# Optimization experiments

Hardware: AMD Instinct MI355X
Metric: run time of the kernel (lower is better)

The kernel has to match this reference:

```python
import jax, jax.numpy as jnp
import numpy as np

WS = 16      # window size
NH = 8       # num heads
LN_EPS = 1e-5
F_NORM_EPS = 1e-12  # torch F.normalize eps


def layer_norm(x, w, b):
    mu = jnp.mean(x, axis=-1, keepdims=True)
    var = jnp.mean((x - mu) ** 2, axis=-1, keepdims=True)
    return (x - mu) / jnp.sqrt(var + LN_EPS) * w + b


def setup_inputs() -> dict:
    key = jax.random.key(0)
    ks = jax.random.split(key, 8)
    b, h, w, c = 2, 192, 192, 128
    n = WS * WS
    x = jax.random.normal(ks[0], (b, h * w, c), dtype=jnp.float32)
    rpi = jax.random.randint(ks[1], (n, n), 0, (2 * WS - 1) ** 2)
    s = 0.02
    inp = {
        'x': x,
        'qkv_w': jax.random.normal(ks[2], (c, 3 * c), jnp.float32) * s,
        'qkv_b': jnp.zeros((3 * c,), jnp.float32),
        'proj_w': jax.random.normal(ks[3], (c, c), jnp.float32) * s,
        'proj_b': jnp.zeros((c,), jnp.float32),
        'logit_scale': jnp.full((NH, 1, 1), jnp.log(10.0), jnp.float32),
        'rpb_table': jax.random.normal(ks[4], ((2 * WS - 1) ** 2, NH), jnp.float32) * s,
        'norm1_w': jnp.ones((c,), jnp.float32),
        'norm1_b': jnp.zeros((c,), jnp.float32),
        'norm2_w': jnp.ones((c,), jnp.float32),
        'norm2_b': jnp.zeros((c,), jnp.float32),
        'fc1_w': jax.random.normal(ks[5], (c, 2 * c), jnp.float32) * s,
        'fc1_b': jnp.zeros((2 * c,), jnp.float32),
        'fc2_w': jax.random.normal(ks[6], (2 * c, c), jnp.float32) * s,
        'fc2_b': jnp.zeros((c,), jnp.float32),
        'h': h,
        'w': w,
        'rpi': rpi,
    }
    return inp


def reference(x, qkv_w, qkv_b, proj_w, proj_b, logit_scale, rpb_table,
              norm1_w, norm1_b, norm2_w, norm2_b, fc1_w, fc1_b, fc2_w, fc2_b,
              h, w, rpi):
    b, L, c = x.shape
    ws, nh = WS, NH
    d = c // nh
    n = ws * ws
    shortcut = x

    # window partition: (b, h, w, c) -> (b*nW, ws*ws, c)
    xi = x.reshape(b, h // ws, ws, w // ws, ws, c)
    xw = xi.transpose(0, 1, 3, 2, 4, 5).reshape(-1, n, c)

    # cosine window attention (SwinV2 style)
    qkv = (xw @ qkv_w + qkv_b).reshape(-1, n, 3, nh, d).transpose(2, 0, 3, 1, 4)
    q, k, v = qkv[0], qkv[1], qkv[2]                       # (B_, nh, n, d)
    qn = q / jnp.maximum(jnp.linalg.norm(q, axis=-1, keepdims=True), F_NORM_EPS)
    kn = k / jnp.maximum(jnp.linalg.norm(k, axis=-1, keepdims=True), F_NORM_EPS)
    scale = jnp.exp(jnp.minimum(logit_scale, jnp.log(100.0)))  # (nh,1,1)
    attn = jnp.einsum('bhnd,bhmd->bhnm', qn, kn) * scale
    bias = rpb_table[rpi.reshape(-1)].reshape(n, n, nh).transpose(2, 0, 1)
    attn = jax.nn.softmax(attn + bias[None], axis=-1)
    out = jnp.einsum('bhnm,bhmd->bhnd', attn, v)
    out = out.transpose(0, 2, 1, 3).reshape(-1, n, c) @ proj_w + proj_b

    # window reverse
    xr = out.reshape(b, h // ws, w // ws, ws, ws, c)
    xr = xr.transpose(0, 1, 3, 2, 4, 5).reshape(b, L, c)

    # res-post-norm residual + MLP (GELU), eval mode (no dropout/drop_path)
    x1 = shortcut + layer_norm(xr, norm1_w, norm1_b)
    y = jax.nn.gelu(x1 @ fc1_w + fc1_b, approximate=False) @ fc2_w + fc2_b
    return x1 + layer_norm(y, norm2_w, norm2_b)
```

## Files before the change

kernel.cpp:

```cpp
#include <hip/hip_runtime.h>
#include <hip/hip_bf16.h>
#include <math.h>

#define BB 2
#define HH 192
#define WW 192
#define CC 128
#define LL (HH*WW)
#define WSZ 16
#define NTOK 256
#define NHEAD 8
#define DHEAD 16
#define NWS 12
#define NWB 144
#define NWT 288
#define MT (BB*LL)

#define OFF_BIAS   0
#define OFF_QKV    262144
#define OFF_ATTN   14417920
#define OFF_X1     19136512
#define OFF_X1B    28573696
#define OFF_HID    33292288
#define OFF_WT     42729472
#define WT_QKV 0
#define WT_PROJ 49152
#define WT_FC1 65536
#define WT_FC2 98304

typedef short  bf16x8 __attribute__((ext_vector_type(8)));
typedef float  f32x4  __attribute__((ext_vector_type(4)));
#define MFMA16(a,b,c) __builtin_amdgcn_mfma_f32_16x16x32_bf16(a,b,c,0,0,0)

__device__ __forceinline__ ushort f2b(float f) {
    uint u = __float_as_uint(f);
    uint r = u + 0x7fffu + ((u >> 16) & 1u);
    return (ushort)(r >> 16);
}
__device__ __forceinline__ float b2f(ushort u) {
    return __uint_as_float(((uint)u) << 16);
}

__device__ __forceinline__ int win_to_g(int wi, int t) {
    int b   = wi / NWB;
    int win = wi - b*NWB;
    int hi  = win / NWS;
    int wj  = win - hi*NWS;
    return b*LL + (hi*WSZ + (t >> 4))*WW + wj*WSZ + (t & 15);
}

__global__ __launch_bounds__(256) void bias_kernel(const int* __restrict__ rpi,
                                                   const float* __restrict__ rpb,
                                                   ushort* __restrict__ biasT) {
    int gid = blockIdx.x*256 + threadIdx.x;
    int j = gid >> 8, i = gid & 255;
    int idx = rpi[i*256 + j];
    #pragma unroll
    for (int h = 0; h < 8; ++h)
        biasT[h*65536 + j*256 + i] = f2b(rpb[idx*8 + h]);
}

__global__ __launch_bounds__(256) void wconv_kernel(const float* __restrict__ qkv_w,
                                                    const float* __restrict__ proj_w,
                                                    const float* __restrict__ fc1_w,
                                                    const float* __restrict__ fc2_w,
                                                    ushort* __restrict__ wt) {
    int gid = blockIdx.x*256 + threadIdx.x;
    if (gid < 49152) {
        int n = gid >> 7, k = gid & 127;
        wt[gid] = f2b(qkv_w[k*384 + n]);
    } else if (gid < 65536) {
        int i = gid - 49152; int n = i >> 7, k = i & 127;
        wt[gid] = f2b(proj_w[k*128 + n]);
    } else if (gid < 98304) {
        int i = gid - 65536; int n = i >> 7, k = i & 127;
        wt[gid] = f2b(fc1_w[k*256 + n]);
    } else {
        int i = gid - 98304; int n = i >> 8, k = i & 255;
        wt[gid] = f2b(fc2_w[k*128 + n]);
    }
}

__global__ __launch_bounds__(256) void qkv_mfma(const float* __restrict__ x,
                                                const ushort* __restrict__ wt,
                                                const float* __restrict__ wb,
                                                const float* __restrict__ lscale,
                                                ushort* __restrict__ qkvbuf) {
    __shared__ ushort alds[128][136];
    const int tid = threadIdx.x;
    const int wi  = blockIdx.x >> 1;
    const int t0w = (blockIdx.x & 1) << 7;
    #pragma unroll
    for (int it = 0; it < 16; ++it) {
        int idx = it*256 + tid;
        int row = idx >> 5, c4 = idx & 31;
        int g = win_to_g(wi, t0w + row);
        float4 v = ((const float4*)x)[g*32 + c4];
        ushort4 b;
        b.x = f2b(v.x); b.y = f2b(v.y); b.z = f2b(v.z); b.w = f2b(v.w);
        *(ushort4*)&alds[row][c4*4] = b;
    }
    __syncthreads();
    const int wv = tid >> 6, lane = tid & 63;
    const int lr = lane & 15, kg = lane >> 4;
    bf16x8 af[2][4];
    #pragma unroll
    for (int mt = 0; mt < 2; ++mt)
        #pragma unroll
        for (int ks = 0; ks < 4; ++ks)
            af[mt][ks] = *(const bf16x8*)&alds[wv*32 + mt*16 + lr][ks*32 + kg*8];

    #pragma unroll 4
    for (int t = 0; t < 24; ++t) {
        bf16x8 bfr[4];
        #pragma unroll
        for (int ks = 0; ks < 4; ++ks)
            bfr[ks] = *(const bf16x8*)(wt + (t*16 + lr)*128 + ks*32 + kg*8);
        f32x4 acc[2];
        acc[0] = (f32x4)0.f; acc[1] = (f32x4)0.f;
        #pragma unroll
        for (int mt = 0; mt < 2; ++mt)
            #pragma unroll
            for (int ks = 0; ks < 4; ++ks)
                acc[mt] = MFMA16(af[mt][ks], bfr[ks], acc[mt]);

        const int s = t >> 3, head = t & 7;
        const float bcol = wb[s*128 + head*16 + lr];
        #pragma unroll
        for (int mt = 0; mt < 2; ++mt)
            #pragma unroll
            for (int r = 0; r < 4; ++r) acc[mt][r] += bcol;
        if (s < 2) {
            float sc = (s == 0) ? __expf(fminf(lscale[head], 4.6051701860f)) : 1.f;
            #pragma unroll
            for (int mt = 0; mt < 2; ++mt)
                #pragma unroll
                for (int r = 0; r < 4; ++r) {
                    float ss = acc[mt][r]*acc[mt][r];
                    ss += __shfl_xor(ss, 1);
                    ss += __shfl_xor(ss, 2);
                    ss += __shfl_xor(ss, 4);
                    ss += __shfl_xor(ss, 8);
                    acc[mt][r] *= sc / fmaxf(sqrtf(ss), 1e-12f);
                }
        }
        ushort* dst = qkvbuf + ((wi*8+head)*3 + s)*4096;
        #pragma unroll
        for (int mt = 0; mt < 2; ++mt)
            #pragma unroll
            for (int r = 0; r < 4; ++r) {
                int row = t0w + wv*32 + mt*16 + kg*4 + r;
                dst[row*16 + lr] = f2b(acc[mt][r]);
            }
    }
}

__global__ __launch_bounds__(256) void attn_mfma(const ushort* __restrict__ qkv,
                                                 const ushort* __restrict__ biasT,
                                                 ushort* __restrict__ attn_o) {
    __shared__ ushort Vt[16][256];
    __shared__ ushort Plds[4][64][72];
    const int tid = threadIdx.x;
    const int wi = blockIdx.x >> 3, head = blockIdx.x & 7;
    const ushort* qb = qkv + ((wi*8 + head)*3)*4096;
    const ushort* kb = qb + 4096;
    const ushort* vb = qb + 8192;
    {
        const ushort* vr = vb + tid*16;
        #pragma unroll
        for (int c = 0; c < 4; ++c) {
            ushort4 vv = *(const ushort4*)(vr + c*4);
            Vt[c*4+0][tid] = vv.x; Vt[c*4+1][tid] = vv.y;
            Vt[c*4+2][tid] = vv.z; Vt[c*4+3][tid] = vv.w;
        }
    }
    const int wv = tid >> 6, lane = tid & 63;
    const int lr = lane & 15, kg = lane >> 4;
    bf16x8 qf[4];
    #pragma unroll
    for (int mt = 0; mt < 4; ++mt)
        qf[mt] = (kg < 2) ? *(const bf16x8*)(qb + (wv*64 + mt*16 + lr)*16 + kg*8)
                          : (bf16x8)0;
    __syncthreads();

    f32x4 oacc[4];
    #pragma unroll
    for (int mt = 0; mt < 4; ++mt) oacc[mt] = (f32x4)0.f;
    float lsum[4][4];
    #pragma unroll
    for (int mt = 0; mt < 4; ++mt)
        #pragma unroll
        for (int r = 0; r < 4; ++r) lsum[mt][r] = 0.f;

    for (int jt = 0; jt < 4; ++jt) {
        bf16x8 kf[4];
        #pragma unroll
        for (int nt = 0; nt < 4; ++nt)
            kf[nt] = (kg < 2) ? *(const bf16x8*)(kb + (jt*64 + nt*16 + lr)*16 + kg*8)
                              : (bf16x8)0;
        #pragma unroll
        for (int nt = 0; nt < 4; ++nt) {
            f32x4 s[4];
            #pragma unroll
            for (int mt = 0; mt < 4; ++mt)
                s[mt] = MFMA16(qf[mt], kf[nt], (f32x4)0.f);
            const int key = jt*64 + nt*16 + lr;
            #pragma unroll
            for (int mt = 0; mt < 4; ++mt) {
                ushort4 bb = *(const ushort4*)(biasT + head*65536 + key*256
                                               + wv*64 + mt*16 + kg*4);
                float p0 = __expf(s[mt][0] + b2f(bb.x));
                float p1 = __expf(s[mt][1] + b2f(bb.y));
                float p2 = __expf(s[mt][2] + b2f(bb.z));
                float p3 = __expf(s[mt][3] + b2f(bb.w));
                lsum[mt][0] += p0; lsum[mt][1] += p1;
                lsum[mt][2] += p2; lsum[mt][3] += p3;
                Plds[wv][mt*16 + kg*4 + 0][nt*16 + lr] = f2b(p0);
                Plds[wv][mt*16 + kg*4 + 1][nt*16 + lr] = f2b(p1);
                Plds[wv][mt*16 + kg*4 + 2][nt*16 + lr] = f2b(p2);
                Plds[wv][mt*16 + kg*4 + 3][nt*16 + lr] = f2b(p3);
            }
        }
        #pragma unroll
        for (int kt = 0; kt < 2; ++kt) {
            bf16x8 vf = *(const bf16x8*)&Vt[lr][jt*64 + kt*32 + kg*8];
            #pragma unroll
            for (int mt = 0; mt < 4; ++mt) {
                bf16x8 pf = *(const bf16x8*)&Plds[wv][mt*16 + lr][kt*32 + kg*8];
                oacc[mt] = MFMA16(pf, vf, oacc[mt]);
            }
        }
    }
    #pragma unroll
    for (int mt = 0; mt < 4; ++mt) {
        #pragma unroll
        for (int r = 0; r < 4; ++r) {
            float v = lsum[mt][r];
            v += __shfl_xor(v, 1);
            v += __shfl_xor(v, 2);
            v += __shfl_xor(v, 4);
            v += __shfl_xor(v, 8);
            lsum[mt][r] = 1.f / v;
        }
    }
    #pragma unroll
    for (int mt = 0; mt < 4; ++mt) {
        #pragma unroll
        for (int r = 0; r < 4; ++r) {
            int q = wv*64 + mt*16 + kg*4 + r;
            attn_o[(wi*256 + q)*128 + head*16 + lr] = f2b(oacc[mt][r] * lsum[mt][r]);
        }
    }
}

__global__ __launch_bounds__(256) void proj_mfma(const ushort* __restrict__ a,
                                                 const ushort* __restrict__ wt,
                                                 const float* __restrict__ wb,
                                                 const float* __restrict__ x,
                                                 const float* __restrict__ n1w,
                                                 const float* __restrict__ n1b,
                                                 float* __restrict__ x1,
                                                 ushort* __restrict__ x1b) {
    __shared__ ushort alds[128][136];
    const int tid = threadIdx.x;
    const int M0 = blockIdx.x * 128;
    #pragma unroll
    for (int it = 0; it < 16; ++it) {
        int idx = it*256 + tid;
        int row = idx >> 5, c4 = idx & 31;
        *(ushort4*)&alds[row][c4*4] = ((const ushort4*)a)[M0*32 + idx];
    }
    __syncthreads();
    const int wv = tid >> 6, lane = tid & 63;
    const int lr = lane & 15, kg = lane >> 4;
    bf16x8 af[2][4];
    #pragma unroll
    for (int mt = 0; mt < 2; ++mt)
        #pragma unroll
        for (int ks = 0; ks < 4; ++ks)
            af[mt][ks] = *(const bf16x8*)&alds[wv*32 + mt*16 + lr][ks*32 + kg*8];

    f32x4 acc[2][8];
    #pragma unroll
    for (int mt = 0; mt < 2; ++mt)
        #pragma unroll
        for (int t = 0; t < 8; ++t) acc[mt][t] = (f32x4)0.f;
    #pragma unroll
    for (int t = 0; t < 8; ++t) {
        bf16x8 bfr[4];
        #pragma unroll
        for (int ks = 0; ks < 4; ++ks)
            bfr[ks] = *(const bf16x8*)(wt + (t*16 + lr)*128 + ks*32 + kg*8);
        #pragma unroll
        for (int mt = 0; mt < 2; ++mt)
            #pragma unroll
            for (int ks = 0; ks < 4; ++ks)
                acc[mt][t] = MFMA16(af[mt][ks], bfr[ks], acc[mt][t]);
    }
    #pragma unroll
    for (int t = 0; t < 8; ++t) {
        float bcol = wb[t*16 + lr];
        #pragma unroll
        for (int mt = 0; mt < 2; ++mt)
            #pragma unroll
            for (int r = 0; r < 4; ++r) acc[mt][t][r] += bcol;
    }
    float mu_[2][4], rs_[2][4];
    #pragma unroll
    for (int mt = 0; mt < 2; ++mt)
        #pragma unroll
        for (int r = 0; r < 4; ++r) {
            float s = 0.f, q = 0.f;
            #pragma unroll
            for (int t = 0; t < 8; ++t) { float v = acc[mt][t][r]; s += v; q += v*v; }
            s += __shfl_xor(s,1); q += __shfl_xor(q,1);
            s += __shfl_xor(s,2); q += __shfl_xor(q,2);
            s += __shfl_xor(s,4); q += __shfl_xor(q,4);
            s += __shfl_xor(s,8); q += __shfl_xor(q,8);
            float mu = s*(1.f/128.f);
            float var = q*(1.f/128.f) - mu*mu;
            mu_[mt][r] = mu; rs_[mt][r] = rsqrtf(var + 1e-5f);
        }
    float w1c[8], b1c[8];
    #pragma unroll
    for (int t = 0; t < 8; ++t) { w1c[t] = n1w[t*16+lr]; b1c[t] = n1b[t*16+lr]; }
    #pragma unroll
    for (int mt = 0; mt < 2; ++mt)
        #pragma unroll
        for (int r = 0; r < 4; ++r) {
            int M = M0 + wv*32 + mt*16 + kg*4 + r;
            int g = win_to_g(M >> 8, M & 255);
            #pragma unroll
            for (int t = 0; t < 8; ++t) {
                int col = t*16 + lr;
                float val = x[g*128 + col]
                          + (acc[mt][t][r]-mu_[mt][r])*rs_[mt][r]*w1c[t] + b1c[t];
                x1[g*128 + col] = val;
                x1b[g*128 + col] = f2b(val);
            }
        }
}

__global__ __launch_bounds__(256) void fc1_mfma(const ushort* __restrict__ a,
                                                const ushort* __restrict__ wt,
                                                const float* __restrict__ wb,
                                                ushort* __restrict__ hidden) {
    __shared__ ushort alds[128][136];
    const int tid = threadIdx.x;
    const int M0 = blockIdx.x * 128;
    #pragma unroll
    for (int it = 0; it < 16; ++it) {
        int idx = it*256 + tid;
        int row = idx >> 5, c4 = idx & 31;
        *(ushort4*)&alds[row][c4*4] = ((const ushort4*)a)[M0*32 + idx];
    }
    __syncthreads();
    const int wv = tid >> 6, lane = tid & 63;
    const int lr = lane & 15, kg = lane >> 4;
    bf16x8 af[2][4];
    #pragma unroll
    for (int mt = 0; mt < 2; ++mt)
        #pragma unroll
        for (int ks = 0; ks < 4; ++ks)
            af[mt][ks] = *(const bf16x8*)&alds[wv*32 + mt*16 + lr][ks*32 + kg*8];

    #pragma unroll 4
    for (int t = 0; t < 16; ++t) {
        bf16x8 bfr[4];
        #pragma unroll
        for (int ks = 0; ks < 4; ++ks)
            bfr[ks] = *(const bf16x8*)(wt + (t*16 + lr)*128 + ks*32 + kg*8);
        f32x4 acc[2];
        acc[0] = (f32x4)0.f; acc[1] = (f32x4)0.f;
        #pragma unroll
        for (int mt = 0; mt < 2; ++mt)
            #pragma unroll
            for (int ks = 0; ks < 4; ++ks)
                acc[mt] = MFMA16(af[mt][ks], bfr[ks], acc[mt]);
        float bcol = wb[t*16 + lr];
        int col = t*16 + lr;
        #pragma unroll
        for (int mt = 0; mt < 2; ++mt)
            #pragma unroll
            for (int r = 0; r < 4; ++r) {
                int row = M0 + wv*32 + mt*16 + kg*4 + r;
                float v = acc[mt][r] + bcol;
                float gl = v*0.5f*(1.f + erff(v*0.70710678118654752f));
                hidden[row*256 + col] = f2b(gl);
            }
    }
}

__global__ __launch_bounds__(256) void fc2_mfma(const ushort* __restrict__ a,
                                                const ushort* __restrict__ wt,
                                                const float* __restrict__ wb,
                                                const float* __restrict__ x1,
                                                const float* __restrict__ n2w,
                                                const float* __restrict__ n2b,
                                                float* __restrict__ out) {
    __shared__ ushort alds[128][136];
    const int tid = threadIdx.x;
    const int M0 = blockIdx.x * 128;
    const int wv = tid >> 6, lane = tid & 63;
    const int lr = lane & 15, kg = lane >> 4;
    f32x4 acc[2][8];
    #pragma unroll
    for (int mt = 0; mt < 2; ++mt)
        #pragma unroll
        for (int t = 0; t < 8; ++t) acc[mt][t] = (f32x4)0.f;

    for (int ko = 0; ko < 2; ++ko) {
        if (ko) __syncthreads();
        #pragma unroll
        for (int it = 0; it < 16; ++it) {
            int idx = it*256 + tid;
            int row = idx >> 5, c4 = idx & 31;
            *(ushort4*)&alds[row][c4*4] =
                *(const ushort4*)(a + (M0+row)*256 + ko*128 + c4*4);
        }
        __syncthreads();
        bf16x8 af[2][4];
        #pragma unroll
        for (int mt = 0; mt < 2; ++mt)
            #pragma unroll
            for (int ks = 0; ks < 4; ++ks)
                af[mt][ks] = *(const bf16x8*)&alds[wv*32 + mt*16 + lr][ks*32 + kg*8];
        #pragma unroll
        for (int t = 0; t < 8; ++t) {
            bf16x8 bfr[4];
            #pragma unroll
            for (int ks = 0; ks < 4; ++ks)
                bfr[ks] = *(const bf16x8*)(wt + (t*16 + lr)*256 + ko*128 + ks*32 + kg*8);
            #pragma unroll
            for (int mt = 0; mt < 2; ++mt)
                #pragma unroll
                for (int ks = 0; ks < 4; ++ks)
                    acc[mt][t] = MFMA16(af[mt][ks], bfr[ks], acc[mt][t]);
        }
    }
    #pragma unroll
    for (int t = 0; t < 8; ++t) {
        float bcol = wb[t*16 + lr];
        #pragma unroll
        for (int mt = 0; mt < 2; ++mt)
            #pragma unroll
            for (int r = 0; r < 4; ++r) acc[mt][t][r] += bcol;
    }
    float mu_[2][4], rs_[2][4];
    #pragma unroll
    for (int mt = 0; mt < 2; ++mt)
        #pragma unroll
        for (int r = 0; r < 4; ++r) {
            float s = 0.f, q = 0.f;
            #pragma unroll
            for (int t = 0; t < 8; ++t) { float v = acc[mt][t][r]; s += v; q += v*v; }
            s += __shfl_xor(s,1); q += __shfl_xor(q,1);
            s += __shfl_xor(s,2); q += __shfl_xor(q,2);
            s += __shfl_xor(s,4); q += __shfl_xor(q,4);
            s += __shfl_xor(s,8); q += __shfl_xor(q,8);
            float mu = s*(1.f/128.f);
            float var = q*(1.f/128.f) - mu*mu;
            mu_[mt][r] = mu; rs_[mt][r] = rsqrtf(var + 1e-5f);
        }
    float w2c[8], b2c[8];
    #pragma unroll
    for (int t = 0; t < 8; ++t) { w2c[t] = n2w[t*16+lr]; b2c[t] = n2b[t*16+lr]; }
    #pragma unroll
    for (int mt = 0; mt < 2; ++mt)
        #pragma unroll
        for (int r = 0; r < 4; ++r) {
            int g = M0 + wv*32 + mt*16 + kg*4 + r;
            #pragma unroll
            for (int t = 0; t < 8; ++t) {
                int col = t*16 + lr;
                out[g*128 + col] = x1[g*128 + col]
                                 + (acc[mt][t][r]-mu_[mt][r])*rs_[mt][r]*w2c[t] + b2c[t];
            }
        }
}

extern "C" void kernel_launch(void* const* d_in, const int* in_sizes, int n_in,
                              void* d_out, int out_size, void* d_ws, size_t ws_size,
                              hipStream_t stream) {
    const float* x      = (const float*)d_in[0];
    const float* qkv_w  = (const float*)d_in[1];
    const float* qkv_b  = (const float*)d_in[2];
    const float* proj_w = (const float*)d_in[3];
    const float* proj_b = (const float*)d_in[4];
    const float* lscale = (const float*)d_in[5];
    const float* rpb    = (const float*)d_in[6];
    const float* n1w    = (const float*)d_in[7];
    const float* n1b    = (const float*)d_in[8];
    const float* n2w    = (const float*)d_in[9];
    const float* n2b    = (const float*)d_in[10];
    const float* fc1_w  = (const float*)d_in[11];
    const float* fc1_b  = (const float*)d_in[12];
    const float* fc2_w  = (const float*)d_in[13];
    const float* fc2_b  = (const float*)d_in[14];
    const int*   rpi    = (const int*)d_in[17];
    float* out = (float*)d_out;

    float* ws      = (float*)d_ws;
    ushort* biasT  = (ushort*)(ws + OFF_BIAS);
    ushort* qkvbuf = (ushort*)(ws + OFF_QKV);
    ushort* attn_o = (ushort*)(ws + OFF_ATTN);
    float*  x1     = ws + OFF_X1;
    ushort* x1b    = (ushort*)(ws + OFF_X1B);
    ushort* hidden = (ushort*)(ws + OFF_HID);
    ushort* wt     = (ushort*)(ws + OFF_WT);

    bias_kernel<<<256, 256, 0, stream>>>(rpi, rpb, biasT);
    wconv_kernel<<<512, 256, 0, stream>>>(qkv_w, proj_w, fc1_w, fc2_w, wt);
    qkv_mfma<<<576, 256, 0, stream>>>(x, wt + WT_QKV, qkv_b, lscale, qkvbuf);
    attn_mfma<<<2304, 256, 0, stream>>>(qkvbuf, biasT, attn_o);
    proj_mfma<<<576, 256, 0, stream>>>(attn_o, wt + WT_PROJ, proj_b, x, n1w, n1b, x1, x1b);
    fc1_mfma<<<576, 256, 0, stream>>>(x1b, wt + WT_FC1, fc1_b, hidden);
    fc2_mfma<<<576, 256, 0, stream>>>(hidden, wt + WT_FC2, fc2_b, x1, n2w, n2b, out);
}
```

Before: 354.7 us.

## Restructure window attention with 32x32 MFMA transposed scores and register-resident P

Rewrites the attention kernel to compute S^T with 32x32x16 bf16 MFMA so each lane's score outputs map directly onto the A-operand layout of the P·V MFMA, removing the LDS round-trip for the probability matrix and the zero-padded K=32 waste in the 16x16x32 QK^T. The exp is switched to exp2 by folding log2(e) into the query scale and the precomputed bias table, and the bias table is now stored non-transposed so each lane reads contiguous bias rows. Row-sum normalisation goes through a small LDS table with an extra barrier. Only half the lanes write the output, and bias loads become per-lane strided global reads.

```diff
diff --git a/kernel.cpp b/kernel.cpp
--- a/kernel.cpp
+++ b/kernel.cpp
@@ -15,6 +15,7 @@
 #define NWB 144
 #define NWT 288
 #define MT (BB*LL)
+#define LOG2E 1.44269504088896340736f
 
 #define OFF_BIAS   0
 #define OFF_QKV    262144
@@ -28,14 +29,21 @@
 #define WT_FC1 65536
 #define WT_FC2 98304
 
-typedef short  bf16x8 __attribute__((ext_vector_type(8)));
-typedef float  f32x4  __attribute__((ext_vector_type(4)));
+typedef short  bf16x8  __attribute__((ext_vector_type(8)));
+typedef short  bf16x4  __attribute__((ext_vector_type(4)));
+typedef float  f32x4   __attribute__((ext_vector_type(4)));
+typedef float  f32x16  __attribute__((ext_vector_type(16)));
+typedef uint   uint4v  __attribute__((ext_vector_type(4)));
 #define MFMA16(a,b,c) __builtin_amdgcn_mfma_f32_16x16x32_bf16(a,b,c,0,0,0)
+#define MFMA32(a,b,c) __builtin_amdgcn_mfma_f32_32x32x16_bf16(a,b,c,0,0,0)
 
 __device__ __forceinline__ ushort f2b(float f) {
     uint u = __float_as_uint(f);
     uint r = u + 0x7fffu + ((u >> 16) & 1u);
     return (ushort)(r >> 16);
+}
+__device__ __forceinline__ uint pk(float a, float b) {
+    return (uint)f2b(a) | ((uint)f2b(b) << 16);
 }
 __device__ __forceinline__ float b2f(ushort u) {
     return __uint_as_float(((uint)u) << 16);
@@ -53,11 +61,11 @@
                                                    const float* __restrict__ rpb,
                                                    ushort* __restrict__ biasT) {
     int gid = blockIdx.x*256 + threadIdx.x;
-    int j = gid >> 8, i = gid & 255;
-    int idx = rpi[i*256 + j];
+    int q = gid >> 8, k = gid & 255;
+    int idx = rpi[q*256 + k];
     #pragma unroll
     for (int h = 0; h < 8; ++h)
-        biasT[h*65536 + j*256 + i] = f2b(rpb[idx*8 + h]);
+        biasT[h*65536 + q*256 + k] = f2b(rpb[idx*8 + h] * LOG2E);
 }
 
 __global__ __launch_bounds__(256) void wconv_kernel(const float* __restrict__ qkv_w,
@@ -131,7 +139,7 @@
             #pragma unroll
             for (int r = 0; r < 4; ++r) acc[mt][r] += bcol;
         if (s < 2) {
-            float sc = (s == 0) ? __expf(fminf(lscale[head], 4.6051701860f)) : 1.f;
+            float sc = (s == 0) ? __expf(fminf(lscale[head], 4.6051701860f)) * LOG2E : 1.f;
             #pragma unroll
             for (int mt = 0; mt < 2; ++mt)
                 #pragma unroll
@@ -158,8 +166,8 @@
 __global__ __launch_bounds__(256) void attn_mfma(const ushort* __restrict__ qkv,
                                                  const ushort* __restrict__ biasT,
                                                  ushort* __restrict__ attn_o) {
-    __shared__ ushort Vt[16][256];
-    __shared__ ushort Plds[4][64][72];
+    __shared__ ushort Vt[16][260];
+    __shared__ float  ltab[4][2][32];
     const int tid = threadIdx.x;
     const int wi = blockIdx.x >> 3, head = blockIdx.x & 7;
     const ushort* qb = qkv + ((wi*8 + head)*3)*4096;
@@ -175,80 +183,80 @@
         }
     }
     const int wv = tid >> 6, lane = tid & 63;
-    const int lr = lane & 15, kg = lane >> 4;
-    bf16x8 qf[4];
-    #pragma unroll
-    for (int mt = 0; mt < 4; ++mt)
-        qf[mt] = (kg < 2) ? *(const bf16x8*)(qb + (wv*64 + mt*16 + lr)*16 + kg*8)
-                          : (bf16x8)0;
+    const int l31 = lane & 31, hi = lane >> 5;
+    const int dp = l31 & 15;
+    bf16x8 qf[2];
+    #pragma unroll
+    for (int mt = 0; mt < 2; ++mt)
+        qf[mt] = *(const bf16x8*)(qb + (wv*64 + mt*32 + l31)*16 + hi*8);
+    const ushort* brow0 = biasT + head*65536 + (wv*64 + l31)*256;
     __syncthreads();
 
-    f32x4 oacc[4];
-    #pragma unroll
-    for (int mt = 0; mt < 4; ++mt) oacc[mt] = (f32x4)0.f;
-    float lsum[4][4];
-    #pragma unroll
-    for (int mt = 0; mt < 4; ++mt)
-        #pragma unroll
-        for (int r = 0; r < 4; ++r) lsum[mt][r] = 0.f;
-
-    for (int jt = 0; jt < 4; ++jt) {
-        bf16x8 kf[4];
-        #pragma unroll
-        for (int nt = 0; nt < 4; ++nt)
-            kf[nt] = (kg < 2) ? *(const bf16x8*)(kb + (jt*64 + nt*16 + lr)*16 + kg*8)
-                              : (bf16x8)0;
-        #pragma unroll
-        for (int nt = 0; nt < 4; ++nt) {
-            f32x4 s[4];
-            #pragma unroll
-            for (int mt = 0; mt < 4; ++mt)
-                s[mt] = MFMA16(qf[mt], kf[nt], (f32x4)0.f);
-            const int key = jt*64 + nt*16 + lr;
-            #pragma unroll
-            for (int mt = 0; mt < 4; ++mt) {
-                ushort4 bb = *(const ushort4*)(biasT + head*65536 + key*256
-                                               + wv*64 + mt*16 + kg*4);
-                float p0 = __expf(s[mt][0] + b2f(bb.x));
-                float p1 = __expf(s[mt][1] + b2f(bb.y));
-                float p2 = __expf(s[mt][2] + b2f(bb.z));
-                float p3 = __expf(s[mt][3] + b2f(bb.w));
-                lsum[mt][0] += p0; lsum[mt][1] += p1;
-                lsum[mt][2] += p2; lsum[mt][3] += p3;
-                Plds[wv][mt*16 + kg*4 + 0][nt*16 + lr] = f2b(p0);
-                Plds[wv][mt*16 + kg*4 + 1][nt*16 + lr] = f2b(p1);
-                Plds[wv][mt*16 + kg*4 + 2][nt*16 + lr] = f2b(p2);
-                Plds[wv][mt*16 + kg*4 + 3][nt*16 + lr] = f2b(p3);
+    f32x16 oacc[2];
+    oacc[0] = (f32x16)0.f; oacc[1] = (f32x16)0.f;
+    float lsum0 = 0.f, lsum1 = 0.f;
+
+    for (int kt = 0; kt < 8; ++kt) {
+        bf16x8 kf = *(const bf16x8*)(kb + (kt*32 + l31)*16 + hi*8);
+        #pragma unroll
+        for (int mt = 0; mt < 2; ++mt) {
+            f32x16 s = MFMA32(kf, qf[mt], (f32x16)0.f);
+            const ushort* br = brow0 + mt*32*256 + kt*32 + 4*hi;
+            ushort4 b0 = *(const ushort4*)(br + 0);
+            ushort4 b1 = *(const ushort4*)(br + 8);
+            ushort4 b2 = *(const ushort4*)(br + 16);
+            ushort4 b3 = *(const ushort4*)(br + 24);
+            float p[16];
+            p[0]  = exp2f(s[0]  + b2f(b0.x));
+            p[1]  = exp2f(s[1]  + b2f(b0.y));
+            p[2]  = exp2f(s[2]  + b2f(b0.z));
+            p[3]  = exp2f(s[3]  + b2f(b0.w));
+            p[4]  = exp2f(s[4]  + b2f(b1.x));
+            p[5]  = exp2f(s[5]  + b2f(b1.y));
+            p[6]  = exp2f(s[6]  + b2f(b1.z));
+            p[7]  = exp2f(s[7]  + b2f(b1.w));
+            p[8]  = exp2f(s[8]  + b2f(b2.x));
+            p[9]  = exp2f(s[9]  + b2f(b2.y));
+            p[10] = exp2f(s[10] + b2f(b2.z));
+            p[11] = exp2f(s[11] + b2f(b2.w));
+            p[12] = exp2f(s[12] + b2f(b3.x));
+            p[13] = exp2f(s[13] + b2f(b3.y));
+            p[14] = exp2f(s[14] + b2f(b3.z));
+            p[15] = exp2f(s[15] + b2f(b3.w));
+            float ls = ((p[0]+p[1])+(p[2]+p[3])) + ((p[4]+p[5])+(p[6]+p[7]))
+                     + ((p[8]+p[9])+(p[10]+p[11])) + ((p[12]+p[13])+(p[14]+p[15]));
+            if (mt == 0) lsum0 += ls; else lsum1 += ls;
+            uint4v t0 = { pk(p[0],p[1]),  pk(p[2],p[3]),  pk(p[4],p[5]),  pk(p[6],p[7])  };
+            uint4v t1 = { pk(p[8],p[9]),  pk(p[10],p[11]),pk(p[12],p[13]),pk(p[14],p[15])};
+            bf16x8 pf0 = __builtin_bit_cast(bf16x8, t0);
+            bf16x8 pf1 = __builtin_bit_cast(bf16x8, t1);
+            bf16x4 v00 = *(const bf16x4*)&Vt[dp][kt*32 + hi*4];
+            bf16x4 v01 = *(const bf16x4*)&Vt[dp][kt*32 + 8 + hi*4];
+            bf16x4 v10 = *(const bf16x4*)&Vt[dp][kt*32 + 16 + hi*4];
+            bf16x4 v11 = *(const bf16x4*)&Vt[dp][kt*32 + 24 + hi*4];
+            bf16x8 vf0 = __builtin_shufflevector(v00, v01, 0,1,2,3,4,5,6,7);
+            bf16x8 vf1 = __builtin_shufflevector(v10, v11, 0,1,2,3,4,5,6,7);
+            oacc[mt] = MFMA32(pf0, vf0, oacc[mt]);
+            oacc[mt] = MFMA32(pf1, vf1, oacc[mt]);
+        }
+    }
+    {
+        float t0 = lsum0 + __shfl_xor(lsum0, 32);
+        float t1 = lsum1 + __shfl_xor(lsum1, 32);
+        ltab[wv][0][l31] = 1.f / t0;
+        ltab[wv][1][l31] = 1.f / t1;
+    }
+    __syncthreads();
+    if (l31 < 16) {
+        #pragma unroll
+        for (int mt = 0; mt < 2; ++mt) {
+            #pragma unroll
+            for (int i = 0; i < 16; ++i) {
+                int q = (i&3) + 8*(i>>2) + 4*hi;
+                float il = ltab[wv][mt][q];
+                attn_o[(wi*256 + wv*64 + mt*32 + q)*128 + head*16 + l31]
+                    = f2b(oacc[mt][i] * il);
             }
-        }
-        #pragma unroll
-        for (int kt = 0; kt < 2; ++kt) {
-            bf16x8 vf = *(const bf16x8*)&Vt[lr][jt*64 + kt*32 + kg*8];
-            #pragma unroll
-            for (int mt = 0; mt < 4; ++mt) {
-                bf16x8 pf = *(const bf16x8*)&Plds[wv][mt*16 + lr][kt*32 + kg*8];
-                oacc[mt] = MFMA16(pf, vf, oacc[mt]);
-            }
-        }
-    }
-    #pragma unroll
-    for (int mt = 0; mt < 4; ++mt) {
-        #pragma unroll
-        for (int r = 0; r < 4; ++r) {
-            float v = lsum[mt][r];
-            v += __shfl_xor(v, 1);
-            v += __shfl_xor(v, 2);
-            v += __shfl_xor(v, 4);
-            v += __shfl_xor(v, 8);
-            lsum[mt][r] = 1.f / v;
-        }
-    }
-    #pragma unroll
-    for (int mt = 0; mt < 4; ++mt) {
-        #pragma unroll
-        for (int r = 0; r < 4; ++r) {
-            int q = wv*64 + mt*16 + kg*4 + r;
-            attn_o[(wi*256 + q)*128 + head*16 + lr] = f2b(oacc[mt][r] * lsum[mt][r]);
         }
     }
 }
```

Result: no change. 353.1 us (-0.5%).
